# Kernel tuning notes

Measured on AMD Instinct MI355X. Metric: run time of the kernel, lower is better.

Reference implementation:

```python
import jax, jax.numpy as jnp
import numpy as np

N_SITE, D, PHYS, W = 40, 128, 2, 8  # sites, MPS bond dim, physical dim, MPO bond dim


def setup_inputs() -> dict:
    key = jax.random.key(0)
    k1, k2 = jax.random.split(key)
    # scale so 40-step transfer-matrix products stay O(1) in float32
    M = jax.random.normal(k1, (N_SITE, D, PHYS, D), jnp.float32) * (D * PHYS) ** -0.5
    H = jax.random.normal(k2, (N_SITE, W, W, PHYS, PHYS), jnp.float32) * (W * PHYS * PHYS) ** -0.5
    return {"M": M, "H": H}


def _energy(M, H):
    # <M|H|M> via left-to-right environment sweep. L has shape (D_bra, w, D_ket).
    L0 = jnp.zeros((D, W, D), M.dtype).at[0, 0, 0].set(1.0)  # open left boundary

    def step(L, mh):
        m, h = mh  # m: (a,i,p) bond,phys,bond ; h: (w,x,i,j) mpo-bond,mpo-bond,phys-out,phys-in
        T = jnp.einsum('awb,aip->wbip', L, m)      # absorb bra tensor (real, so no conj)
        T = jnp.einsum('wbip,wxij->bpxj', T, h)    # absorb MPO tensor
        L = jnp.einsum('bpxj,bjq->pxq', T, m)      # absorb ket tensor
        return L, None

    L, _ = jax.lax.scan(step, L0, (M, H))
    return L[0, W - 1, 0]  # open right boundary (MPO right boundary = last index)


def _norm(M):
    # <M|M> via transfer-matrix sweep. N has shape (D_bra, D_ket); stays PSD.
    N0 = jnp.zeros((D, D), M.dtype).at[0, 0].set(1.0)

    def step(N, m):
        T = jnp.einsum('ab,aip->bip', N, m)
        N = jnp.einsum('bip,biq->pq', T, m)
        return N, None

    N, _ = jax.lax.scan(step, N0, M)
    return N[0, 0]


def reference(M, H):
    EPS = 0.0
    NORM_LIM = 10000.0
    energy = _energy(M, H)
    norm = _norm(M)
    loss = energy / (norm + EPS)  # torch.real is identity for real dtype
    reg = jax.nn.relu(norm - NORM_LIM)
    return (energy, norm, loss, reg)
```

## Files before the change

### kernel.cpp

```cpp
#include <hip/hip_runtime.h>


#define D 128
#define W 8
#define NS 40
#define NPAIR 20
#define HALF2 10
#define MSZ (D * 2 * D)
#define HSZ (W * W * 2 * 2)
#define M2SZ (D * 4 * D)
#define H2SZ (W * W * 4 * 4)
#define LSZ (D * W * D)
#define NSZ (D * D)
#define T2SZ (D * W * D * 4)
#define TNSZ (4 * D * D)

#define OFF_M2 0
#define OFF_MR2 (OFF_M2 + NPAIR * M2SZ)
#define OFF_H2 (OFF_MR2 + HALF2 * M2SZ)
#define OFF_HR2 (OFF_H2 + NPAIR * H2SZ)
#define OFF_LL (OFF_HR2 + HALF2 * H2SZ)
#define OFF_LR (OFF_LL + LSZ)
#define OFF_NL (OFF_LR + LSZ)
#define OFF_NR (OFF_NL + NSZ)
#define OFF_T2L (OFF_NR + NSZ)
#define OFF_T2R (OFF_T2L + T2SZ)
#define OFF_TNL (OFF_T2R + T2SZ)
#define OFF_TNR (OFF_TNL + TNSZ)
#define OFF_PART (OFF_TNR + TNSZ)
#define OFF_PARTN (OFF_PART + 128)

__global__ __launch_bounds__(256) void k_prep1(const float* __restrict__ Min,
                                               const float* __restrict__ Hin,
                                               float* __restrict__ ws) {
    __shared__ float As[32 * 34];
    __shared__ float Bs[32 * 68];
    int bid = blockIdx.x, t = threadIdx.x;
    if (bid < 640) {
        int m = bid >> 5, tile = bid & 31;
        int r0 = (tile & 7) * 32, c0 = (tile >> 3) * 64;
        const float* A = Min + (2 * m) * MSZ;
        const float* B = Min + (2 * m + 1) * MSZ;
        float* C = ws + OFF_M2 + m * M2SZ;
        int ty = t >> 4, tx = t & 15;
        float a00 = 0, a01 = 0, a02 = 0, a03 = 0;
        float a10 = 0, a11 = 0, a12 = 0, a13 = 0;
        for (int c = 0; c < 4; ++c) {
            int k0 = c * 32;
            __syncthreads();
            {
                int rr = t >> 3, kq = t & 7;
                int row = r0 + rr;
                const float4 v = *(const float4*)&A[(row >> 1) * 256 + (row & 1) * 128 + k0 + kq * 4];
                float* dst = &As[kq * 136 + rr];
                dst[0] = v.x; dst[34] = v.y; dst[68] = v.z; dst[102] = v.w;
            }
#pragma unroll
            for (int u = 0; u < 2; ++u) {
                int e = u * 256 + t;
                int kk = e >> 4, cq = e & 15;
                const float4 v = *(const float4*)&B[(k0 + kk) * 256 + c0 + cq * 4];
                *(float4*)&Bs[kk * 68 + cq * 4] = v;
            }
            __syncthreads();
#pragma unroll 8
            for (int kk = 0; kk < 32; ++kk) {
                float2 av = *(float2*)&As[kk * 34 + 2 * ty];
                float4 bv = *(float4*)&Bs[kk * 68 + 4 * tx];
                a00 += av.x * bv.x; a01 += av.x * bv.y; a02 += av.x * bv.z; a03 += av.x * bv.w;
                a10 += av.y * bv.x; a11 += av.y * bv.y; a12 += av.y * bv.z; a13 += av.y * bv.w;
            }
        }
        int r = r0 + 2 * ty, cc = c0 + 4 * tx;
        int a = r >> 1, i2 = cc >> 7, cd = cc & 127;
        float4 v0; v0.x = a00; v0.y = a01; v0.z = a02; v0.w = a03;
        float4 v1; v1.x = a10; v1.y = a11; v1.z = a12; v1.w = a13;
        *(float4*)&C[a * 512 + (0 * 2 + i2) * 128 + cd] = v0;
        *(float4*)&C[a * 512 + (1 * 2 + i2) * 128 + cd] = v1;
    } else {
        for (int idx = t; idx < NPAIR * H2SZ; idx += 256) {
            int m = idx >> 10, r = idx & 1023;
            int w = r >> 7, x = (r >> 4) & 7, I = (r >> 2) & 3, J = r & 3;
            int i1 = I >> 1, i2 = I & 1, j1 = J >> 1, j2 = J & 1;
            const float* Ha = Hin + (2 * m) * HSZ;
            const float* Hb = Hin + (2 * m + 1) * HSZ;
            float s = 0.f;
#pragma unroll
            for (int v = 0; v < 8; ++v)
                s += Ha[w * 32 + v * 4 + i1 * 2 + j1] * Hb[v * 32 + x * 4 + i2 * 2 + j2];
            ws[OFF_H2 + idx] = s;
        }
    }
}

#define PR_MR (HALF2 * M2SZ)
#define PR_HR (PR_MR + HALF2 * H2SZ)
#define PR_TOT (PR_HR + 2 * LSZ + 2 * NSZ)
__global__ __launch_bounds__(256) void k_prep2(float* __restrict__ ws) {
    for (int idx = blockIdx.x * 256 + threadIdx.x; idx < PR_TOT; idx += gridDim.x * 256) {
        if (idx < PR_MR) {
            int kr = idx >> 16, r = idx & 65535;
            int a = r >> 9, I = (r >> 7) & 3, p = r & 127;
            ws[OFF_MR2 + idx] = ws[OFF_M2 + (19 - kr) * M2SZ + p * 512 + I * 128 + a];
        } else if (idx < PR_HR) {
            int e = idx - PR_MR;
            int kr = e >> 10, r = e & 1023;
            int w = r >> 7, x = (r >> 4) & 7, lo = r & 15;
            ws[OFF_HR2 + e] = ws[OFF_H2 + (19 - kr) * H2SZ + x * 128 + w * 16 + lo];
        } else {
            int e = idx - PR_HR;
            int off; float v = 0.f;
            if (e < LSZ)            { off = OFF_LL + e; if (e == 0) v = 1.f; }
            else if (e < 2 * LSZ)   { int r = e - LSZ; off = OFF_LR + r; if (r == (W - 1) * D) v = 1.f; }
            else if (e < 2 * LSZ + NSZ) { int r = e - 2 * LSZ; off = OFF_NL + r; if (r == 0) v = 1.f; }
            else                    { int r = e - 2 * LSZ - NSZ; off = OFF_NR + r; if (r == 0) v = 1.f; }
            ws[off] = v;
        }
    }
}

__global__ __launch_bounds__(256) void k_A2(const float* __restrict__ ws_c,
                                            float* __restrict__ ws, int k) {
    __shared__ float sm[9472];
    (void)ws_c;
    int bid = blockIdx.x, t = threadIdx.x;
    if (bid < 128) {
        int side = bid >> 6;
        int eb = bid & 63;
        int b0 = (eb & 7) * 16;
        int p0 = (eb >> 3) * 16;
        const float* Lsrc = ws + (side ? OFF_LR : OFF_LL);
        const float* m2 = ws + (side ? OFF_MR2 : OFF_M2) + k * M2SZ;
        const float* h2 = ws + (side ? OFF_HR2 : OFF_H2) + k * H2SZ;
        float* T2 = ws + (side ? OFF_T2R : OFF_T2L);
        float* Ls = sm;
        float* ms = sm + 6400;
        float* hs = sm + 8448;
#pragma unroll
        for (int u = 0; u < 4; ++u) {
            int e = u * 256 + t;
            int w = e >> 7, I = (e >> 5) & 3, x = (e >> 2) & 7, J = e & 3;
            hs[e] = h2[w * 128 + x * 16 + I * 4 + J];
        }
        int b_l = t & 15, p_l = t >> 4;
        float acc[8][4];
#pragma unroll
        for (int w = 0; w < 8; ++w)
#pragma unroll
            for (int I = 0; I < 4; ++I) acc[w][I] = 0.f;
        for (int c = 0; c < 4; ++c) {
            int a0 = c * 32;
            __syncthreads();
#pragma unroll
            for (int u = 0; u < 4; ++u) {
                int e = u * 256 + t;
                int aa = e >> 5, w = (e >> 2) & 7, bq = e & 3;
                const float4 v = *(const float4*)&Lsrc[(a0 + aa) * 1024 + w * 128 + b0 + bq * 4];
                float* dst = &Ls[aa * 200 + bq * 48 + w];
                dst[0] = v.x; dst[12] = v.y; dst[24] = v.z; dst[36] = v.w;
            }
#pragma unroll
            for (int u = 0; u < 2; ++u) {
                int s = u * 256 + t;
                int aa = s >> 4, I = (s >> 2) & 3, pq = s & 3;
                const float4 v = *(const float4*)&m2[(a0 + aa) * 512 + I * 128 + p0 + pq * 4];
                *(float4*)&ms[aa * 64 + I * 16 + pq * 4] = v;
            }
            __syncthreads();
#pragma unroll 4
            for (int aa = 0; aa < 32; ++aa) {
                float4 l0 = *(float4*)&Ls[aa * 200 + b_l * 12];
                float4 l1 = *(float4*)&Ls[aa * 200 + b_l * 12 + 4];
                float lw[8] = {l0.x, l0.y, l0.z, l0.w, l1.x, l1.y, l1.z, l1.w};
                float mv[4];
#pragma unroll
                for (int I = 0; I < 4; ++I) mv[I] = ms[aa * 64 + I * 16 + p_l];
#pragma unroll
                for (int w = 0; w < 8; ++w)
#pragma unroll
                    for (int I = 0; I < 4; ++I) acc[w][I] += lw[w] * mv[I];
            }
        }
        float o[32];
#pragma unroll
        for (int xJ = 0; xJ < 32; ++xJ) o[xJ] = 0.f;
#pragma unroll
        for (int wI = 0; wI < 32; ++wI) {
            float tv = acc[wI >> 2][wI & 3];
#pragma unroll
            for (int xJ = 0; xJ < 32; ++xJ) o[xJ] += tv * hs[wI * 32 + xJ];
        }
        int b = b0 + b_l, p = p0 + p_l;
#pragma unroll
        for (int x = 0; x < 8; ++x) {
            float4 v; v.x = o[x * 4]; v.y = o[x * 4 + 1]; v.z = o[x * 4 + 2]; v.w = o[x * 4 + 3];
            *(float4*)&T2[p * 4096 + x * 512 + b * 4] = v;
        }
    } else {
        int nb = bid - 128;
        int side = nb >> 5;
        int nn = nb & 31;
        int b0 = (nn & 3) * 32;
        int c0 = (nn >> 2) * 64;
        const float* Nsrc = ws + (side ? OFF_NR : OFF_NL);
        const float* m2 = ws + (side ? OFF_MR2 : OFF_M2) + k * M2SZ;
        float* Tn = ws + (side ? OFF_TNR : OFF_TNL);
        float* As = sm;
        float* Bs = sm + 1056;
        int ty = t >> 4, tx = t & 15;
        float a00 = 0, a01 = 0, a02 = 0, a03 = 0;
        float a10 = 0, a11 = 0, a12 = 0, a13 = 0;
        for (int c = 0; c < 4; ++c) {
            int a0 = c * 32;
            __syncthreads();
#pragma unroll
            for (int u = 0; u < 4; ++u) {
                int e = u * 256 + t;
                int kk = e >> 5, col = e & 31;
                As[kk * 33 + col] = Nsrc[(a0 + kk) * 128 + b0 + col];
            }
#pragma unroll
            for (int u = 0; u < 8; ++u) {
                int e = u * 256 + t;
                int kk = e >> 6, col = e & 63;
                Bs[kk * 68 + col] = m2[(a0 + kk) * 512 + c0 + col];
            }
            __syncthreads();
#pragma unroll 8
            for (int kk = 0; kk < 32; ++kk) {
                float2 av = *(float2*)&As[kk * 33 + 2 * ty];
                float4 bv = *(float4*)&Bs[kk * 68 + 4 * tx];
                a00 += av.x * bv.x; a01 += av.x * bv.y; a02 += av.x * bv.z; a03 += av.x * bv.w;
                a10 += av.y * bv.x; a11 += av.y * bv.y; a12 += av.y * bv.z; a13 += av.y * bv.w;
            }
        }
        int b_ = b0 + 2 * ty;
        float rowv[2][4] = {{a00, a01, a02, a03}, {a10, a11, a12, a13}};
#pragma unroll
        for (int jj = 0; jj < 4; ++jj) {
            int col = c0 + 4 * tx + jj;
            int I = col >> 7, p = col & 127;
            Tn[I * 16384 + p * 128 + b_] = rowv[0][jj];
            Tn[I * 16384 + p * 128 + b_ + 1] = rowv[1][jj];
        }
    }
}

__global__ __launch_bounds__(256) void k_B2(float* __restrict__ ws, int k) {
    __shared__ float As[32 * 34];
    __shared__ float Bs[32 * 68];
    int bid = blockIdx.x, t = threadIdx.x;
    int ty = t >> 4, tx = t & 15;
    float a00 = 0, a01 = 0, a02 = 0, a03 = 0;
    float a10 = 0, a11 = 0, a12 = 0, a13 = 0;
    if (bid < 128) {
        int side = bid >> 6;
        int eb = bid & 63;
        int r0 = (eb & 31) * 32;
        int c0 = (eb >> 5) * 64;
        const float* A = ws + (side ? OFF_T2R : OFF_T2L);
        const float* B = ws + (side ? OFF_MR2 : OFF_M2) + k * M2SZ;
        float* C = ws + (side ? OFF_LR : OFF_LL);
        for (int c = 0; c < 16; ++c) {
            int k0 = c * 32;
            __syncthreads();
            {
                int rr = t >> 3, kq = t & 7;
                const float4 v = *(const float4*)&A[(r0 + rr) * 512 + k0 + kq * 4];
                float* dst = &As[kq * 136 + rr];
                dst[0] = v.x; dst[34] = v.y; dst[68] = v.z; dst[102] = v.w;
            }
#pragma unroll
            for (int u = 0; u < 2; ++u) {
                int e = u * 256 + t;
                int kk = e >> 4, cq = e & 15;
                int row = k0 + kk;
                const float4 v = *(const float4*)&B[(row >> 2) * 512 + (row & 3) * 128 + c0 + cq * 4];
                *(float4*)&Bs[kk * 68 + cq * 4] = v;
            }
            __syncthreads();
#pragma unroll 8
            for (int kk = 0; kk < 32; ++kk) {
                float2 av = *(float2*)&As[kk * 34 + 2 * ty];
                float4 bv = *(float4*)&Bs[kk * 68 + 4 * tx];
                a00 += av.x * bv.x; a01 += av.x * bv.y; a02 += av.x * bv.z; a03 += av.x * bv.w;
                a10 += av.y * bv.x; a11 += av.y * bv.y; a12 += av.y * bv.z; a13 += av.y * bv.w;
            }
        }
        int r = r0 + 2 * ty, cc = c0 + 4 * tx;
        float4 v0; v0.x = a00; v0.y = a01; v0.z = a02; v0.w = a03;
        float4 v1; v1.x = a10; v1.y = a11; v1.z = a12; v1.w = a13;
        *(float4*)&C[(r >> 3) * 1024 + (r & 7) * 128 + cc] = v0;
        *(float4*)&C[((r + 1) >> 3) * 1024 + ((r + 1) & 7) * 128 + cc] = v1;
    } else if (bid < 144) {
        int nb = bid - 128;
        int side = nb >> 3;
        int nn = nb & 7;
        int r0 = (nn & 3) * 32;
        int c0 = (nn >> 2) * 64;
        const float* A = ws + (side ? OFF_TNR : OFF_TNL);
        const float* B = ws + (side ? OFF_MR2 : OFF_M2) + k * M2SZ;
        float* C = ws + (side ? OFF_NR : OFF_NL);
        for (int c = 0; c < 16; ++c) {
            int k0 = c * 32;
            int Ic = k0 >> 7, bc = k0 & 127;
            __syncthreads();
            {
                int rr = t >> 3, kq = t & 7;
                const float4 v = *(const float4*)&A[Ic * 16384 + (r0 + rr) * 128 + bc + kq * 4];
                float* dst = &As[kq * 136 + rr];
                dst[0] = v.x; dst[34] = v.y; dst[68] = v.z; dst[102] = v.w;
            }
#pragma unroll
            for (int u = 0; u < 2; ++u) {
                int e = u * 256 + t;
                int kk = e >> 4, cq = e & 15;
                const float4 v = *(const float4*)&B[(bc + kk) * 512 + Ic * 128 + c0 + cq * 4];
                *(float4*)&Bs[kk * 68 + cq * 4] = v;
            }
            __syncthreads();
#pragma unroll 8
            for (int kk = 0; kk < 32; ++kk) {
                float2 av = *(float2*)&As[kk * 34 + 2 * ty];
                float4 bv = *(float4*)&Bs[kk * 68 + 4 * tx];
                a00 += av.x * bv.x; a01 += av.x * bv.y; a02 += av.x * bv.z; a03 += av.x * bv.w;
                a10 += av.y * bv.x; a11 += av.y * bv.y; a12 += av.y * bv.z; a13 += av.y * bv.w;
            }
        }
        int r = r0 + 2 * ty, cc = c0 + 4 * tx;
        float4 v0; v0.x = a00; v0.y = a01; v0.z = a02; v0.w = a03;
        float4 v1; v1.x = a10; v1.y = a11; v1.z = a12; v1.w = a13;
        *(float4*)&C[r * 128 + cc] = v0;
        *(float4*)&C[(r + 1) * 128 + cc] = v1;
    }
}

__global__ __launch_bounds__(256) void k_dot(float* __restrict__ ws) {
    __shared__ float se[256], sn[256];
    int bid = blockIdx.x, t = threadIdx.x;
    const float* LL = ws + OFF_LL;
    const float* LR = ws + OFF_LR;
    float e = 0.f;
#pragma unroll
    for (int u = 0; u < 4; ++u) {
        int i = bid * 1024 + u * 256 + t;
        e += LL[i] * LR[i];
    }
    float n = 0.f;
    if (t < 128) {
        int i = bid * 128 + t;
        n = ws[OFF_NL + i] * ws[OFF_NR + i];
    }
    se[t] = e;
    sn[t] = n;
    __syncthreads();
    for (int s = 128; s > 0; s >>= 1) {
        if (t < s) { se[t] += se[t + s]; sn[t] += sn[t + s]; }
        __syncthreads();
    }
    if (t == 0) {
        ws[OFF_PART + bid] = se[0];
        ws[OFF_PARTN + bid] = sn[0];
    }
}

__global__ __launch_bounds__(256) void k_loss(const float* __restrict__ ws,
                                              float* __restrict__ out) {
    __shared__ float se[128], sn[128];
    int t = threadIdx.x;
    if (t < 128) {
        se[t] = ws[OFF_PART + t];
        sn[t] = ws[OFF_PARTN + t];
    }
    __syncthreads();
    for (int s = 64; s > 0; s >>= 1) {
        if (t < s) { se[t] += se[t + s]; sn[t] += sn[t + s]; }
        __syncthreads();
    }
    if (t == 0) {
        float E = se[0], Nm = sn[0];
        out[0] = E;
        out[1] = Nm;
        out[2] = E / Nm;
        out[3] = fmaxf(Nm - 10000.0f, 0.0f);
    }
}

extern "C" void kernel_launch(void* const* d_in, const int* in_sizes, int n_in,
                              void* d_out, int out_size, void* d_ws, size_t ws_size,
                              hipStream_t stream) {
    const float* Min = (const float*)d_in[0];
    const float* Hin = (const float*)d_in[1];
    float* ws = (float*)d_ws;
    float* out = (float*)d_out;
    (void)in_sizes; (void)n_in; (void)out_size; (void)ws_size;

    k_prep1<<<dim3(641), dim3(256), 0, stream>>>(Min, Hin, ws);
    k_prep2<<<dim3(640), dim3(256), 0, stream>>>(ws);
    for (int k = 0; k < HALF2; ++k) {
        k_A2<<<dim3(192), dim3(256), 0, stream>>>(ws, ws, k);
        k_B2<<<dim3(144), dim3(256), 0, stream>>>(ws, k);
    }
    k_dot<<<dim3(128), dim3(256), 0, stream>>>(ws);
    k_loss<<<dim3(1), dim3(256), 0, stream>>>(ws, out);
}
```

Baseline: 476.8 us.

## Fuse whole sweep into one persistent kernel with software grid barriers

Replaces the chain of about two dozen kernel launches (prep, ten A/B step pairs, dot, loss) with a single persistent kernel of 256 blocks. Stages are separated by custom global barriers using relaxed atomics, an XCD-aware writeback fence, and sc0 loads that bypass stale cache. The norm-sweep tasks are re-tiled and the B stages use larger K chunks. The aim is to remove launch gaps between dependent steps, at the cost of relying on co-residency of all blocks and on hand-written cache-coherence handling that could be fragile.

```diff
diff --git a/kernel.cpp b/kernel.cpp
--- a/kernel.cpp
+++ b/kernel.cpp
@@ -28,16 +28,112 @@
 #define OFF_TNL (OFF_T2R + T2SZ)
 #define OFF_TNR (OFF_TNL + TNSZ)
 #define OFF_PART (OFF_TNR + TNSZ)
-#define OFF_PARTN (OFF_PART + 128)
-
-__global__ __launch_bounds__(256) void k_prep1(const float* __restrict__ Min,
-                                               const float* __restrict__ Hin,
-                                               float* __restrict__ ws) {
-    __shared__ float As[32 * 34];
-    __shared__ float Bs[32 * 68];
-    int bid = blockIdx.x, t = threadIdx.x;
-    if (bid < 640) {
-        int m = bid >> 5, tile = bid & 31;
+#define OFF_PARTN (OFF_PART + 128 * 32)
+#define WS_FLOATS (OFF_PARTN + 128 * 32)
+
+#define NBLK 256
+#define OFF_BAR WS_FLOATS
+#define BAR_CLEAN (32 * NBLK)
+#define BAR_CNT (BAR_CLEAN + 32 * 8)
+#define BAR_LCTR (BAR_CNT + 32 * 8)
+#define BAR_INTS (BAR_LCTR + 32 * 4)
+
+#define PR2_TOT (HALF2 * M2SZ + HALF2 * H2SZ)
+
+typedef float f32x4_t __attribute__((ext_vector_type(4)));
+
+__device__ __forceinline__ int ld_rlx(int* p) {
+    return __hip_atomic_load(p, __ATOMIC_RELAXED, __HIP_MEMORY_SCOPE_AGENT);
+}
+__device__ __forceinline__ void st_rlx(int* p, int v) {
+    __hip_atomic_store(p, v, __ATOMIC_RELAXED, __HIP_MEMORY_SCOPE_AGENT);
+}
+__device__ __forceinline__ int fadd_rlx(int* p, int v) {
+    return __hip_atomic_fetch_add(p, v, __ATOMIC_RELAXED, __HIP_MEMORY_SCOPE_AGENT);
+}
+
+__device__ __forceinline__ float ld_sc0(const float* p) {
+    float v;
+    asm volatile("global_load_dword %0, %1, off sc0\n\ts_waitcnt vmcnt(0)"
+                 : "=&v"(v) : "v"(p) : "memory");
+    return v;
+}
+__device__ __forceinline__ void ld1x4_sc0(const float* p0, const float* p1,
+                                          const float* p2, const float* p3,
+                                          float& v0, float& v1, float& v2, float& v3) {
+    asm volatile(
+        "global_load_dword %0, %4, off sc0\n\t"
+        "global_load_dword %1, %5, off sc0\n\t"
+        "global_load_dword %2, %6, off sc0\n\t"
+        "global_load_dword %3, %7, off sc0\n\t"
+        "s_waitcnt vmcnt(0)"
+        : "=&v"(v0), "=&v"(v1), "=&v"(v2), "=&v"(v3)
+        : "v"(p0), "v"(p1), "v"(p2), "v"(p3) : "memory");
+}
+__device__ __forceinline__ void ld4x2_sc0(const float* p0, const float* p1,
+                                          f32x4_t& v0, f32x4_t& v1) {
+    asm volatile(
+        "global_load_dwordx4 %0, %2, off sc0\n\t"
+        "global_load_dwordx4 %1, %3, off sc0\n\t"
+        "s_waitcnt vmcnt(0)"
+        : "=&v"(v0), "=&v"(v1) : "v"(p0), "v"(p1) : "memory");
+}
+__device__ __forceinline__ void ld4x4_sc0(const float* p0, const float* p1,
+                                          const float* p2, const float* p3,
+                                          f32x4_t& v0, f32x4_t& v1,
+                                          f32x4_t& v2, f32x4_t& v3) {
+    asm volatile(
+        "global_load_dwordx4 %0, %4, off sc0\n\t"
+        "global_load_dwordx4 %1, %5, off sc0\n\t"
+        "global_load_dwordx4 %2, %6, off sc0\n\t"
+        "global_load_dwordx4 %3, %7, off sc0\n\t"
+        "s_waitcnt vmcnt(0)"
+        : "=&v"(v0), "=&v"(v1), "=&v"(v2), "=&v"(v3)
+        : "v"(p0), "v"(p1), "v"(p2), "v"(p3) : "memory");
+}
+
+__global__ __launch_bounds__(256) void k_bzero(float* ws) {
+    int idx = blockIdx.x * 256 + threadIdx.x;
+    int* bar = (int*)(ws + OFF_BAR);
+    if (idx < BAR_INTS) bar[idx] = 0;
+}
+
+__device__ void gbar(int* bar, int ep, bool wb, int isLead, int myxcd,
+                     unsigned presMask) {
+    int t = threadIdx.x;
+    asm volatile("s_waitcnt vmcnt(0)" ::: "memory");
+    __syncthreads();
+    if (t == 0) st_rlx(&bar[32 * blockIdx.x], ep);
+    while (ld_rlx(&bar[32 * t]) < ep) __builtin_amdgcn_s_sleep(2);
+    __syncthreads();
+    if (wb) {
+        if (isLead && t == 0) {
+            __builtin_amdgcn_fence(__ATOMIC_RELEASE, "agent");
+            st_rlx(&bar[BAR_CLEAN + 32 * myxcd], ep);
+        }
+        if (t < 8 && ((presMask >> t) & 1)) {
+            while (ld_rlx(&bar[BAR_CLEAN + 32 * t]) < ep) __builtin_amdgcn_s_sleep(2);
+        }
+        __syncthreads();
+    }
+}
+
+__device__ __forceinline__ void lbar(int* lc, int target) {
+    asm volatile("s_waitcnt vmcnt(0)" ::: "memory");
+    __syncthreads();
+    if (threadIdx.x == 0) {
+        fadd_rlx(lc, 1);
+        while (ld_rlx(lc) < target) __builtin_amdgcn_s_sleep(2);
+    }
+    __syncthreads();
+}
+
+__device__ void prep1_task(int task, const float* Min, const float* Hin,
+                           float* ws, float* sm, int t) {
+    if (task < 640) {
+        float* As = sm;
+        float* Bs = sm + 1088;
+        int m = task >> 5, tile = task & 31;
         int r0 = (tile & 7) * 32, c0 = (tile >> 3) * 64;
         const float* A = Min + (2 * m) * MSZ;
         const float* B = Min + (2 * m + 1) * MSZ;
@@ -51,7 +147,7 @@
             {
                 int rr = t >> 3, kq = t & 7;
                 int row = r0 + rr;
-                const float4 v = *(const float4*)&A[(row >> 1) * 256 + (row & 1) * 128 + k0 + kq * 4];
+                const f32x4_t v = *(const f32x4_t*)&A[(row >> 1) * 256 + (row & 1) * 128 + k0 + kq * 4];
                 float* dst = &As[kq * 136 + rr];
                 dst[0] = v.x; dst[34] = v.y; dst[68] = v.z; dst[102] = v.w;
             }
@@ -59,26 +155,27 @@
             for (int u = 0; u < 2; ++u) {
                 int e = u * 256 + t;
                 int kk = e >> 4, cq = e & 15;
-                const float4 v = *(const float4*)&B[(k0 + kk) * 256 + c0 + cq * 4];
-                *(float4*)&Bs[kk * 68 + cq * 4] = v;
+                const f32x4_t v = *(const f32x4_t*)&B[(k0 + kk) * 256 + c0 + cq * 4];
+                *(f32x4_t*)&Bs[kk * 68 + cq * 4] = v;
             }
             __syncthreads();
 #pragma unroll 8
             for (int kk = 0; kk < 32; ++kk) {
-                float2 av = *(float2*)&As[kk * 34 + 2 * ty];
-                float4 bv = *(float4*)&Bs[kk * 68 + 4 * tx];
-                a00 += av.x * bv.x; a01 += av.x * bv.y; a02 += av.x * bv.z; a03 += av.x * bv.w;
-                a10 += av.y * bv.x; a11 += av.y * bv.y; a12 += av.y * bv.z; a13 += av.y * bv.w;
+                float av0 = As[kk * 34 + 2 * ty], av1 = As[kk * 34 + 2 * ty + 1];
+                f32x4_t bv = *(const f32x4_t*)&Bs[kk * 68 + 4 * tx];
+                a00 += av0 * bv.x; a01 += av0 * bv.y; a02 += av0 * bv.z; a03 += av0 * bv.w;
+                a10 += av1 * bv.x; a11 += av1 * bv.y; a12 += av1 * bv.z; a13 += av1 * bv.w;
             }
         }
         int r = r0 + 2 * ty, cc = c0 + 4 * tx;
         int a = r >> 1, i2 = cc >> 7, cd = cc & 127;
-        float4 v0; v0.x = a00; v0.y = a01; v0.z = a02; v0.w = a03;
-        float4 v1; v1.x = a10; v1.y = a11; v1.z = a12; v1.w = a13;
-        *(float4*)&C[a * 512 + (0 * 2 + i2) * 128 + cd] = v0;
-        *(float4*)&C[a * 512 + (1 * 2 + i2) * 128 + cd] = v1;
+        f32x4_t v0; v0.x = a00; v0.y = a01; v0.z = a02; v0.w = a03;
+        f32x4_t v1; v1.x = a10; v1.y = a11; v1.z = a12; v1.w = a13;
+        *(f32x4_t*)&C[a * 512 + (0 * 2 + i2) * 128 + cd] = v0;
+        *(f32x4_t*)&C[a * 512 + (1 * 2 + i2) * 128 + cd] = v1;
     } else {
-        for (int idx = t; idx < NPAIR * H2SZ; idx += 256) {
+        int chunk = task - 640;
+        for (int idx = chunk * 1280 + t; idx < (chunk + 1) * 1280; idx += 256) {
             int m = idx >> 10, r = idx & 1023;
             int w = r >> 7, x = (r >> 4) & 7, I = (r >> 2) & 3, J = r & 3;
             int i1 = I >> 1, i2 = I & 1, j1 = J >> 1, j2 = J & 1;
@@ -93,296 +190,382 @@
     }
 }
 
-#define PR_MR (HALF2 * M2SZ)
-#define PR_HR (PR_MR + HALF2 * H2SZ)
-#define PR_TOT (PR_HR + 2 * LSZ + 2 * NSZ)
-__global__ __launch_bounds__(256) void k_prep2(float* __restrict__ ws) {
-    for (int idx = blockIdx.x * 256 + threadIdx.x; idx < PR_TOT; idx += gridDim.x * 256) {
-        if (idx < PR_MR) {
+__device__ void eA_task(int eb, const float* L, const float* m2, const float* h2,
+                        float* T2, float* sm, int t) {
+    int b0 = (eb & 7) * 16;
+    int p0 = (eb >> 3) * 16;
+    float* Ls = sm;
+    float* ms = sm + 6400;
+    float* hs = sm + 8448;
+    __syncthreads();
+#pragma unroll
+    for (int u = 0; u < 4; ++u) {
+        int e = u * 256 + t;
+        int w = e >> 7, I = (e >> 5) & 3, x = (e >> 2) & 7, J = e & 3;
+        hs[e] = h2[w * 128 + x * 16 + I * 4 + J];
+    }
+    int b_l = t & 15, p_l = t >> 4;
+    float acc[8][4];
+#pragma unroll
+    for (int w = 0; w < 8; ++w)
+#pragma unroll
+        for (int I = 0; I < 4; ++I) acc[w][I] = 0.f;
+    for (int c = 0; c < 4; ++c) {
+        int a0 = c * 32;
+        __syncthreads();
+        {
+            int e0 = t, e1 = 256 + t, e2 = 512 + t, e3 = 768 + t;
+            const float* q0 = &L[(a0 + (e0 >> 5)) * 1024 + ((e0 >> 2) & 7) * 128 + b0 + (e0 & 3) * 4];
+            const float* q1 = &L[(a0 + (e1 >> 5)) * 1024 + ((e1 >> 2) & 7) * 128 + b0 + (e1 & 3) * 4];
+            const float* q2 = &L[(a0 + (e2 >> 5)) * 1024 + ((e2 >> 2) & 7) * 128 + b0 + (e2 & 3) * 4];
+            const float* q3 = &L[(a0 + (e3 >> 5)) * 1024 + ((e3 >> 2) & 7) * 128 + b0 + (e3 & 3) * 4];
+            f32x4_t v0, v1, v2, v3;
+            ld4x4_sc0(q0, q1, q2, q3, v0, v1, v2, v3);
+            float* d0 = &Ls[(e0 >> 5) * 200 + (e0 & 3) * 48 + ((e0 >> 2) & 7)];
+            d0[0] = v0.x; d0[12] = v0.y; d0[24] = v0.z; d0[36] = v0.w;
+            float* d1 = &Ls[(e1 >> 5) * 200 + (e1 & 3) * 48 + ((e1 >> 2) & 7)];
+            d1[0] = v1.x; d1[12] = v1.y; d1[24] = v1.z; d1[36] = v1.w;
+            float* d2 = &Ls[(e2 >> 5) * 200 + (e2 & 3) * 48 + ((e2 >> 2) & 7)];
+            d2[0] = v2.x; d2[12] = v2.y; d2[24] = v2.z; d2[36] = v2.w;
+            float* d3 = &Ls[(e3 >> 5) * 200 + (e3 & 3) * 48 + ((e3 >> 2) & 7)];
+            d3[0] = v3.x; d3[12] = v3.y; d3[24] = v3.z; d3[36] = v3.w;
+        }
+#pragma unroll
+        for (int u = 0; u < 2; ++u) {
+            int s = u * 256 + t;
+            int aa = s >> 4, I = (s >> 2) & 3, pq = s & 3;
+            const f32x4_t v = *(const f32x4_t*)&m2[(a0 + aa) * 512 + I * 128 + p0 + pq * 4];
+            *(f32x4_t*)&ms[aa * 64 + I * 16 + pq * 4] = v;
+        }
+        __syncthreads();
+#pragma unroll 4
+        for (int aa = 0; aa < 32; ++aa) {
+            f32x4_t l0 = *(const f32x4_t*)&Ls[aa * 200 + b_l * 12];
+            f32x4_t l1 = *(const f32x4_t*)&Ls[aa * 200 + b_l * 12 + 4];
+            float lw[8] = {l0.x, l0.y, l0.z, l0.w, l1.x, l1.y, l1.z, l1.w};
+            float mv[4];
+#pragma unroll
+            for (int I = 0; I < 4; ++I) mv[I] = ms[aa * 64 + I * 16 + p_l];
+#pragma unroll
+            for (int w = 0; w < 8; ++w)
+#pragma unroll
+                for (int I = 0; I < 4; ++I) acc[w][I] += lw[w] * mv[I];
+        }
+    }
+    float o[32];
+#pragma unroll
+    for (int xJ = 0; xJ < 32; ++xJ) o[xJ] = 0.f;
+#pragma unroll
+    for (int wI = 0; wI < 32; ++wI) {
+        float tv = acc[wI >> 2][wI & 3];
+#pragma unroll
+        for (int xJ = 0; xJ < 32; ++xJ) o[xJ] += tv * hs[wI * 32 + xJ];
+    }
+    int b = b0 + b_l, p = p0 + p_l;
+#pragma unroll
+    for (int x = 0; x < 8; ++x) {
+        f32x4_t v; v.x = o[x * 4]; v.y = o[x * 4 + 1]; v.z = o[x * 4 + 2]; v.w = o[x * 4 + 3];
+        *(f32x4_t*)&T2[p * 4096 + x * 512 + b * 4] = v;
+    }
+}
+
+__device__ void eB_task(int eb, const float* T2A, const float* m2, float* Lout,
+                        float* sm, int t) {
+    float* As = sm;
+    float* Bs = sm + 2176;
+    int r0 = (eb & 31) * 32;
+    int c0 = (eb >> 5) * 64;
+    int ty = t >> 4, tx = t & 15;
+    float a00 = 0, a01 = 0, a02 = 0, a03 = 0;
+    float a10 = 0, a11 = 0, a12 = 0, a13 = 0;
+    for (int c = 0; c < 8; ++c) {
+        int k0 = c * 64;
+        __syncthreads();
+        {
+            int rr = t >> 3, kq = t & 7;
+            const float* p0 = &T2A[(r0 + rr) * 512 + k0 + kq * 4];
+            const float* p1 = p0 + 32;
+            f32x4_t v0, v1;
+            ld4x2_sc0(p0, p1, v0, v1);
+            float* d0 = &As[kq * 136 + rr];
+            d0[0] = v0.x; d0[34] = v0.y; d0[68] = v0.z; d0[102] = v0.w;
+            float* d1 = &As[(kq + 8) * 136 + rr];
+            d1[0] = v1.x; d1[34] = v1.y; d1[68] = v1.z; d1[102] = v1.w;
+        }
+#pragma unroll
+        for (int u = 0; u < 4; ++u) {
+            int e = u * 256 + t;
+            int kk = e >> 4, cq = e & 15;
+            int row = k0 + kk;
+            const f32x4_t v = *(const f32x4_t*)&m2[(row >> 2) * 512 + (row & 3) * 128 + c0 + cq * 4];
+            *(f32x4_t*)&Bs[kk * 68 + cq * 4] = v;
+        }
+        __syncthreads();
+#pragma unroll 8
+        for (int kk = 0; kk < 64; ++kk) {
+            float av0 = As[kk * 34 + 2 * ty], av1 = As[kk * 34 + 2 * ty + 1];
+            f32x4_t bv = *(const f32x4_t*)&Bs[kk * 68 + 4 * tx];
+            a00 += av0 * bv.x; a01 += av0 * bv.y; a02 += av0 * bv.z; a03 += av0 * bv.w;
+            a10 += av1 * bv.x; a11 += av1 * bv.y; a12 += av1 * bv.z; a13 += av1 * bv.w;
+        }
+    }
+    int r = r0 + 2 * ty, cc = c0 + 4 * tx;
+    f32x4_t v0; v0.x = a00; v0.y = a01; v0.z = a02; v0.w = a03;
+    f32x4_t v1; v1.x = a10; v1.y = a11; v1.z = a12; v1.w = a13;
+    *(f32x4_t*)&Lout[(r >> 3) * 1024 + (r & 7) * 128 + cc] = v0;
+    *(f32x4_t*)&Lout[((r + 1) >> 3) * 1024 + ((r + 1) & 7) * 128 + cc] = v1;
+}
+
+__device__ void nA_task(int nn, const float* N, const float* m2, float* Tn,
+                        float* sm, int t) {
+    float* As = sm;
+    float* Bs = sm + 1056;
+    int b0 = (nn & 3) * 32;
+    int c0 = (nn >> 2) * 64;
+    int ty = t >> 4, tx = t & 15;
+    float a00 = 0, a01 = 0, a02 = 0, a03 = 0;
+    float a10 = 0, a11 = 0, a12 = 0, a13 = 0;
+    for (int c = 0; c < 4; ++c) {
+        int a0 = c * 32;
+        __syncthreads();
+        {
+            int e0 = t, e1 = 256 + t, e2 = 512 + t, e3 = 768 + t;
+            const float* q0 = &N[(a0 + (e0 >> 5)) * 128 + b0 + (e0 & 31)];
+            const float* q1 = &N[(a0 + (e1 >> 5)) * 128 + b0 + (e1 & 31)];
+            const float* q2 = &N[(a0 + (e2 >> 5)) * 128 + b0 + (e2 & 31)];
+            const float* q3 = &N[(a0 + (e3 >> 5)) * 128 + b0 + (e3 & 31)];
+            float f0, f1, f2, f3;
+            ld1x4_sc0(q0, q1, q2, q3, f0, f1, f2, f3);
+            As[(e0 >> 5) * 33 + (e0 & 31)] = f0;
+            As[(e1 >> 5) * 33 + (e1 & 31)] = f1;
+            As[(e2 >> 5) * 33 + (e2 & 31)] = f2;
+            As[(e3 >> 5) * 33 + (e3 & 31)] = f3;
+        }
+#pragma unroll
+        for (int u = 0; u < 2; ++u) {
+            int e = u * 256 + t;
+            int kk = e >> 4, cq = e & 15;
+            const f32x4_t v = *(const f32x4_t*)&m2[(a0 + kk) * 512 + c0 + cq * 4];
+            *(f32x4_t*)&Bs[kk * 68 + cq * 4] = v;
+        }
+        __syncthreads();
+#pragma unroll 8
+        for (int kk = 0; kk < 32; ++kk) {
+            float av0 = As[kk * 33 + 2 * ty], av1 = As[kk * 33 + 2 * ty + 1];
+            f32x4_t bv = *(const f32x4_t*)&Bs[kk * 68 + 4 * tx];
+            a00 += av0 * bv.x; a01 += av0 * bv.y; a02 += av0 * bv.z; a03 += av0 * bv.w;
+            a10 += av1 * bv.x; a11 += av1 * bv.y; a12 += av1 * bv.z; a13 += av1 * bv.w;
+        }
+    }
+    int b_ = b0 + 2 * ty;
+    float rowv[2][4] = {{a00, a01, a02, a03}, {a10, a11, a12, a13}};
+#pragma unroll
+    for (int jj = 0; jj < 4; ++jj) {
+        int col = c0 + 4 * tx + jj;
+        int I = col >> 7, p = col & 127;
+        Tn[I * 16384 + p * 128 + b_] = rowv[0][jj];
+        Tn[I * 16384 + p * 128 + b_ + 1] = rowv[1][jj];
+    }
+}
+
+__device__ void nB_task(int nn, const float* Tn, const float* m2, float* Nout,
+                        float* sm, int t) {
+    float* As = sm;
+    float* Bs = sm + 2176;
+    int r0 = (nn & 3) * 32;
+    int c0 = (nn >> 2) * 64;
+    int ty = t >> 4, tx = t & 15;
+    float a00 = 0, a01 = 0, a02 = 0, a03 = 0;
+    float a10 = 0, a11 = 0, a12 = 0, a13 = 0;
+    for (int c = 0; c < 8; ++c) {
+        int Ic = c >> 1, bc = (c & 1) * 64;
+        __syncthreads();
+        {
+            int rr = t >> 3, kq = t & 7;
+            const float* p0 = &Tn[Ic * 16384 + (r0 + rr) * 128 + bc + kq * 4];
+            const float* p1 = p0 + 32;
+            f32x4_t v0, v1;
+            ld4x2_sc0(p0, p1, v0, v1);
+            float* d0 = &As[kq * 136 + rr];
+            d0[0] = v0.x; d0[34] = v0.y; d0[68] = v0.z; d0[102] = v0.w;
+            float* d1 = &As[(kq + 8) * 136 + rr];
+            d1[0] = v1.x; d1[34] = v1.y; d1[68] = v1.z; d1[102] = v1.w;
+        }
+#pragma unroll
+        for (int u = 0; u < 4; ++u) {
+            int e = u * 256 + t;
+            int kk = e >> 4, cq = e & 15;
+            const f32x4_t v = *(const f32x4_t*)&m2[(bc + kk) * 512 + Ic * 128 + c0 + cq * 4];
+            *(f32x4_t*)&Bs[kk * 68 + cq * 4] = v;
+        }
+        __syncthreads();
+#pragma unroll 8
+        for (int kk = 0; kk < 64; ++kk) {
+            float av0 = As[kk * 34 + 2 * ty], av1 = As[kk * 34 + 2 * ty + 1];
+            f32x4_t bv = *(const f32x4_t*)&Bs[kk * 68 + 4 * tx];
+            a00 += av0 * bv.x; a01 += av0 * bv.y; a02 += av0 * bv.z; a03 += av0 * bv.w;
+            a10 += av1 * bv.x; a11 += av1 * bv.y; a12 += av1 * bv.z; a13 += av1 * bv.w;
+        }
+    }
+    int r = r0 + 2 * ty, cc = c0 + 4 * tx;
+    f32x4_t v0; v0.x = a00; v0.y = a01; v0.z = a02; v0.w = a03;
+    f32x4_t v1; v1.x = a10; v1.y = a11; v1.z = a12; v1.w = a13;
+    *(f32x4_t*)&Nout[r * 128 + cc] = v0;
+    *(f32x4_t*)&Nout[(r + 1) * 128 + cc] = v1;
+}
+
+__global__ __launch_bounds__(256) void k_sweep(const float* __restrict__ Min,
+                                               const float* __restrict__ Hin,
+                                               float* __restrict__ ws,
+                                               float* __restrict__ out) {
+    __shared__ __align__(16) float sm[9472];
+    __shared__ int shI[12];
+    int* bar = (int*)(ws + OFF_BAR);
+    const int bid = blockIdx.x;
+    const int t = threadIdx.x;
+
+    if (t == 0) {
+        int x;
+        asm volatile("s_getreg_b32 %0, hwreg(HW_REG_XCC_ID)" : "=s"(x));
+        x &= 7;
+        int r = fadd_rlx(&bar[BAR_CNT + 32 * x], 1);
+        shI[0] = x; shI[1] = r;
+    }
+    __syncthreads();
+    const int myxcd = shI[0], rank = shI[1];
+
+    gbar(bar, 1, false, 0, 0, 0);
+
+    if (t == 0) {
+        int pres[8]; unsigned pm = 0; int np = 0;
+        for (int x = 0; x < 8; ++x) {
+            int c = ld_rlx(&bar[BAR_CNT + 32 * x]);
+            if (x == myxcd) shI[2] = c;
+            if (c > 0) { pres[np++] = x; pm |= 1u << x; }
+        }
+        shI[3] = (rank == 0);
+        shI[4] = (int)pm;
+        int nmc = 0;
+        for (int c = 0; c < 4; ++c)
+            if (pres[c % np] == myxcd) shI[6 + nmc++] = c;
+        shI[5] = nmc;
+    }
+    __syncthreads();
+    const int n_g = shI[2], isLead = shI[3];
+    const unsigned presMask = (unsigned)shI[4];
+    const int nMyChains = shI[5];
+
+    for (int task = bid; task < 656; task += NBLK)
+        prep1_task(task, Min, Hin, ws, sm, t);
+    gbar(bar, 2, true, isLead, myxcd, presMask);
+
+    for (int idx = bid * 256 + t; idx < PR2_TOT; idx += NBLK * 256) {
+        if (idx < HALF2 * M2SZ) {
             int kr = idx >> 16, r = idx & 65535;
             int a = r >> 9, I = (r >> 7) & 3, p = r & 127;
             ws[OFF_MR2 + idx] = ws[OFF_M2 + (19 - kr) * M2SZ + p * 512 + I * 128 + a];
-        } else if (idx < PR_HR) {
-            int e = idx - PR_MR;
+        } else {
+            int e = idx - HALF2 * M2SZ;
             int kr = e >> 10, r = e & 1023;
             int w = r >> 7, x = (r >> 4) & 7, lo = r & 15;
             ws[OFF_HR2 + e] = ws[OFF_H2 + (19 - kr) * H2SZ + x * 128 + w * 16 + lo];
+        }
+    }
+    gbar(bar, 3, true, isLead, myxcd, presMask);
+
+    for (int ci = 0; ci < nMyChains; ++ci) {
+        int chain = shI[6 + ci];
+        int* lc = &bar[BAR_LCTR + 32 * chain];
+        int lep = 0;
+        int side = chain & 1;
+        if (chain < 2) {
+            float* L = ws + (side ? OFF_LR : OFF_LL);
+            const float* m2b = ws + (side ? OFF_MR2 : OFF_M2);
+            const float* h2b = ws + (side ? OFF_HR2 : OFF_H2);
+            float* T2 = ws + (side ? OFF_T2R : OFF_T2L);
+            int hot = side ? (W - 1) * D : 0;
+            for (int i = rank * 256 + t; i < LSZ; i += n_g * 256)
+                L[i] = (i == hot) ? 1.f : 0.f;
+            ++lep; lbar(lc, lep * n_g);
+            for (int k = 0; k < HALF2; ++k) {
+                const float* m2 = m2b + k * M2SZ;
+                const float* h2 = h2b + k * H2SZ;
+                for (int task = rank; task < 64; task += n_g)
+                    eA_task(task, L, m2, h2, T2, sm, t);
+                ++lep; lbar(lc, lep * n_g);
+                for (int task = rank; task < 64; task += n_g)
+                    eB_task(task, T2, m2, L, sm, t);
+                ++lep; lbar(lc, lep * n_g);
+            }
         } else {
-            int e = idx - PR_HR;
-            int off; float v = 0.f;
-            if (e < LSZ)            { off = OFF_LL + e; if (e == 0) v = 1.f; }
-            else if (e < 2 * LSZ)   { int r = e - LSZ; off = OFF_LR + r; if (r == (W - 1) * D) v = 1.f; }
-            else if (e < 2 * LSZ + NSZ) { int r = e - 2 * LSZ; off = OFF_NL + r; if (r == 0) v = 1.f; }
-            else                    { int r = e - 2 * LSZ - NSZ; off = OFF_NR + r; if (r == 0) v = 1.f; }
-            ws[off] = v;
-        }
-    }
-}
-
-__global__ __launch_bounds__(256) void k_A2(const float* __restrict__ ws_c,
-                                            float* __restrict__ ws, int k) {
-    __shared__ float sm[9472];
-    (void)ws_c;
-    int bid = blockIdx.x, t = threadIdx.x;
+            float* N = ws + (side ? OFF_NR : OFF_NL);
+            const float* m2b = ws + (side ? OFF_MR2 : OFF_M2);
+            float* Tn = ws + (side ? OFF_TNR : OFF_TNL);
+            for (int i = rank * 256 + t; i < NSZ; i += n_g * 256)
+                N[i] = (i == 0) ? 1.f : 0.f;
+            ++lep; lbar(lc, lep * n_g);
+            for (int k = 0; k < HALF2; ++k) {
+                const float* m2 = m2b + k * M2SZ;
+                for (int task = rank; task < 32; task += n_g)
+                    nA_task(task, N, m2, Tn, sm, t);
+                ++lep; lbar(lc, lep * n_g);
+                for (int task = rank; task < 8; task += n_g)
+                    nB_task(task, Tn, m2, N, sm, t);
+                ++lep; lbar(lc, lep * n_g);
+            }
+        }
+    }
+    gbar(bar, 4, true, isLead, myxcd, presMask);
+
     if (bid < 128) {
-        int side = bid >> 6;
-        int eb = bid & 63;
-        int b0 = (eb & 7) * 16;
-        int p0 = (eb >> 3) * 16;
-        const float* Lsrc = ws + (side ? OFF_LR : OFF_LL);
-        const float* m2 = ws + (side ? OFF_MR2 : OFF_M2) + k * M2SZ;
-        const float* h2 = ws + (side ? OFF_HR2 : OFF_H2) + k * H2SZ;
-        float* T2 = ws + (side ? OFF_T2R : OFF_T2L);
-        float* Ls = sm;
-        float* ms = sm + 6400;
-        float* hs = sm + 8448;
+        float* se = sm;
+        float* sn = sm + 256;
+        const float* LL = ws + OFF_LL;
+        const float* LR = ws + OFF_LR;
+        float e = 0.f;
 #pragma unroll
         for (int u = 0; u < 4; ++u) {
-            int e = u * 256 + t;
-            int w = e >> 7, I = (e >> 5) & 3, x = (e >> 2) & 7, J = e & 3;
-            hs[e] = h2[w * 128 + x * 16 + I * 4 + J];
-        }
-        int b_l = t & 15, p_l = t >> 4;
-        float acc[8][4];
-#pragma unroll
-        for (int w = 0; w < 8; ++w)
-#pragma unroll
-            for (int I = 0; I < 4; ++I) acc[w][I] = 0.f;
-        for (int c = 0; c < 4; ++c) {
-            int a0 = c * 32;
+            int i = bid * 1024 + u * 256 + t;
+            e += ld_sc0(&LL[i]) * ld_sc0(&LR[i]);
+        }
+        float n = 0.f;
+        if (t < 128) {
+            int i = bid * 128 + t;
+            n = ld_sc0(&ws[OFF_NL + i]) * ld_sc0(&ws[OFF_NR + i]);
+        }
+        se[t] = e;
+        sn[t] = n;
+        __syncthreads();
+        for (int s = 128; s > 0; s >>= 1) {
+            if (t < s) { se[t] += se[t + s]; sn[t] += sn[t + s]; }
             __syncthreads();
-#pragma unroll
-            for (int u = 0; u < 4; ++u) {
-                int e = u * 256 + t;
-                int aa = e >> 5, w = (e >> 2) & 7, bq = e & 3;
-                const float4 v = *(const float4*)&Lsrc[(a0 + aa) * 1024 + w * 128 + b0 + bq * 4];
-                float* dst = &Ls[aa * 200 + bq * 48 + w];
-                dst[0] = v.x; dst[12] = v.y; dst[24] = v.z; dst[36] = v.w;
-            }
-#pragma unroll
-            for (int u = 0; u < 2; ++u) {
-                int s = u * 256 + t;
-                int aa = s >> 4, I = (s >> 2) & 3, pq = s & 3;
-                const float4 v = *(const float4*)&m2[(a0 + aa) * 512 + I * 128 + p0 + pq * 4];
-                *(float4*)&ms[aa * 64 + I * 16 + pq * 4] = v;
-            }
+        }
+        if (t == 0) {
+            ws[OFF_PART + bid * 32] = se[0];
+            ws[OFF_PARTN + bid * 32] = sn[0];
+        }
+    }
+    gbar(bar, 5, true, isLead, myxcd, presMask);
+
+    if (bid == 0) {
+        float* se = sm;
+        float* sn = sm + 128;
+        if (t < 128) {
+            se[t] = ws[OFF_PART + t * 32];
+            sn[t] = ws[OFF_PARTN + t * 32];
+        }
+        __syncthreads();
+        for (int s = 64; s > 0; s >>= 1) {
+            if (t < s) { se[t] += se[t + s]; sn[t] += sn[t + s]; }
             __syncthreads();
-#pragma unroll 4
-            for (int aa = 0; aa < 32; ++aa) {
-                float4 l0 = *(float4*)&Ls[aa * 200 + b_l * 12];
-                float4 l1 = *(float4*)&Ls[aa * 200 + b_l * 12 + 4];
-                float lw[8] = {l0.x, l0.y, l0.z, l0.w, l1.x, l1.y, l1.z, l1.w};
-                float mv[4];
-#pragma unroll
-                for (int I = 0; I < 4; ++I) mv[I] = ms[aa * 64 + I * 16 + p_l];
-#pragma unroll
-                for (int w = 0; w < 8; ++w)
-#pragma unroll
-                    for (int I = 0; I < 4; ++I) acc[w][I] += lw[w] * mv[I];
-            }
-        }
-        float o[32];
-#pragma unroll
-        for (int xJ = 0; xJ < 32; ++xJ) o[xJ] = 0.f;
-#pragma unroll
-        for (int wI = 0; wI < 32; ++wI) {
-            float tv = acc[wI >> 2][wI & 3];
-#pragma unroll
-            for (int xJ = 0; xJ < 32; ++xJ) o[xJ] += tv * hs[wI * 32 + xJ];
-        }
-        int b = b0 + b_l, p = p0 + p_l;
-#pragma unroll
-        for (int x = 0; x < 8; ++x) {
-            float4 v; v.x = o[x * 4]; v.y = o[x * 4 + 1]; v.z = o[x * 4 + 2]; v.w = o[x * 4 + 3];
-            *(float4*)&T2[p * 4096 + x * 512 + b * 4] = v;
-        }
-    } else {
-        int nb = bid - 128;
-        int side = nb >> 5;
-        int nn = nb & 31;
-        int b0 = (nn & 3) * 32;
-        int c0 = (nn >> 2) * 64;
-        const float* Nsrc = ws + (side ? OFF_NR : OFF_NL);
-        const float* m2 = ws + (side ? OFF_MR2 : OFF_M2) + k * M2SZ;
-        float* Tn = ws + (side ? OFF_TNR : OFF_TNL);
-        float* As = sm;
-        float* Bs = sm + 1056;
-        int ty = t >> 4, tx = t & 15;
-        float a00 = 0, a01 = 0, a02 = 0, a03 = 0;
-        float a10 = 0, a11 = 0, a12 = 0, a13 = 0;
-        for (int c = 0; c < 4; ++c) {
-            int a0 = c * 32;
-            __syncthreads();
-#pragma unroll
-            for (int u = 0; u < 4; ++u) {
-                int e = u * 256 + t;
-                int kk = e >> 5, col = e & 31;
-                As[kk * 33 + col] = Nsrc[(a0 + kk) * 128 + b0 + col];
-            }
-#pragma unroll
-            for (int u = 0; u < 8; ++u) {
-                int e = u * 256 + t;
-                int kk = e >> 6, col = e & 63;
-                Bs[kk * 68 + col] = m2[(a0 + kk) * 512 + c0 + col];
-            }
-            __syncthreads();
-#pragma unroll 8
-            for (int kk = 0; kk < 32; ++kk) {
-                float2 av = *(float2*)&As[kk * 33 + 2 * ty];
-                float4 bv = *(float4*)&Bs[kk * 68 + 4 * tx];
-                a00 += av.x * bv.x; a01 += av.x * bv.y; a02 += av.x * bv.z; a03 += av.x * bv.w;
-                a10 += av.y * bv.x; a11 += av.y * bv.y; a12 += av.y * bv.z; a13 += av.y * bv.w;
-            }
-        }
-        int b_ = b0 + 2 * ty;
-        float rowv[2][4] = {{a00, a01, a02, a03}, {a10, a11, a12, a13}};
-#pragma unroll
-        for (int jj = 0; jj < 4; ++jj) {
-            int col = c0 + 4 * tx + jj;
-            int I = col >> 7, p = col & 127;
-            Tn[I * 16384 + p * 128 + b_] = rowv[0][jj];
-            Tn[I * 16384 + p * 128 + b_ + 1] = rowv[1][jj];
-        }
-    }
-}
-
-__global__ __launch_bounds__(256) void k_B2(float* __restrict__ ws, int k) {
-    __shared__ float As[32 * 34];
-    __shared__ float Bs[32 * 68];
-    int bid = blockIdx.x, t = threadIdx.x;
-    int ty = t >> 4, tx = t & 15;
-    float a00 = 0, a01 = 0, a02 = 0, a03 = 0;
-    float a10 = 0, a11 = 0, a12 = 0, a13 = 0;
-    if (bid < 128) {
-        int side = bid >> 6;
-        int eb = bid & 63;
-        int r0 = (eb & 31) * 32;
-        int c0 = (eb >> 5) * 64;
-        const float* A = ws + (side ? OFF_T2R : OFF_T2L);
-        const float* B = ws + (side ? OFF_MR2 : OFF_M2) + k * M2SZ;
-        float* C = ws + (side ? OFF_LR : OFF_LL);
-        for (int c = 0; c < 16; ++c) {
-            int k0 = c * 32;
-            __syncthreads();
-            {
-                int rr = t >> 3, kq = t & 7;
-                const float4 v = *(const float4*)&A[(r0 + rr) * 512 + k0 + kq * 4];
-                float* dst = &As[kq * 136 + rr];
-                dst[0] = v.x; dst[34] = v.y; dst[68] = v.z; dst[102] = v.w;
-            }
-#pragma unroll
-            for (int u = 0; u < 2; ++u) {
-                int e = u * 256 + t;
-                int kk = e >> 4, cq = e & 15;
-                int row = k0 + kk;
-                const float4 v = *(const float4*)&B[(row >> 2) * 512 + (row & 3) * 128 + c0 + cq * 4];
-                *(float4*)&Bs[kk * 68 + cq * 4] = v;
-            }
-            __syncthreads();
-#pragma unroll 8
-            for (int kk = 0; kk < 32; ++kk) {
-                float2 av = *(float2*)&As[kk * 34 + 2 * ty];
-                float4 bv = *(float4*)&Bs[kk * 68 + 4 * tx];
-                a00 += av.x * bv.x; a01 += av.x * bv.y; a02 += av.x * bv.z; a03 += av.x * bv.w;
-                a10 += av.y * bv.x; a11 += av.y * bv.y; a12 += av.y * bv.z; a13 += av.y * bv.w;
-            }
-        }
-        int r = r0 + 2 * ty, cc = c0 + 4 * tx;
-        float4 v0; v0.x = a00; v0.y = a01; v0.z = a02; v0.w = a03;
-        float4 v1; v1.x = a10; v1.y = a11; v1.z = a12; v1.w = a13;
-        *(float4*)&C[(r >> 3) * 1024 + (r & 7) * 128 + cc] = v0;
-        *(float4*)&C[((r + 1) >> 3) * 1024 + ((r + 1) & 7) * 128 + cc] = v1;
-    } else if (bid < 144) {
-        int nb = bid - 128;
-        int side = nb >> 3;
-        int nn = nb & 7;
-        int r0 = (nn & 3) * 32;
-        int c0 = (nn >> 2) * 64;
-        const float* A = ws + (side ? OFF_TNR : OFF_TNL);
-        const float* B = ws + (side ? OFF_MR2 : OFF_M2) + k * M2SZ;
-        float* C = ws + (side ? OFF_NR : OFF_NL);
-        for (int c = 0; c < 16; ++c) {
-            int k0 = c * 32;
-            int Ic = k0 >> 7, bc = k0 & 127;
-            __syncthreads();
-            {
-                int rr = t >> 3, kq = t & 7;
-                const float4 v = *(const float4*)&A[Ic * 16384 + (r0 + rr) * 128 + bc + kq * 4];
-                float* dst = &As[kq * 136 + rr];
-                dst[0] = v.x; dst[34] = v.y; dst[68] = v.z; dst[102] = v.w;
-            }
-#pragma unroll
-            for (int u = 0; u < 2; ++u) {
-                int e = u * 256 + t;
-                int kk = e >> 4, cq = e & 15;
-                const float4 v = *(const float4*)&B[(bc + kk) * 512 + Ic * 128 + c0 + cq * 4];
-                *(float4*)&Bs[kk * 68 + cq * 4] = v;
-            }
-            __syncthreads();
-#pragma unroll 8
-            for (int kk = 0; kk < 32; ++kk) {
-                float2 av = *(float2*)&As[kk * 34 + 2 * ty];
-                float4 bv = *(float4*)&Bs[kk * 68 + 4 * tx];
-                a00 += av.x * bv.x; a01 += av.x * bv.y; a02 += av.x * bv.z; a03 += av.x * bv.w;
-                a10 += av.y * bv.x; a11 += av.y * bv.y; a12 += av.y * bv.z; a13 += av.y * bv.w;
-            }
-        }
-        int r = r0 + 2 * ty, cc = c0 + 4 * tx;
-        float4 v0; v0.x = a00; v0.y = a01; v0.z = a02; v0.w = a03;
-        float4 v1; v1.x = a10; v1.y = a11; v1.z = a12; v1.w = a13;
-        *(float4*)&C[r * 128 + cc] = v0;
-        *(float4*)&C[(r + 1) * 128 + cc] = v1;
-    }
-}
-
-__global__ __launch_bounds__(256) void k_dot(float* __restrict__ ws) {
-    __shared__ float se[256], sn[256];
-    int bid = blockIdx.x, t = threadIdx.x;
-    const float* LL = ws + OFF_LL;
-    const float* LR = ws + OFF_LR;
-    float e = 0.f;
-#pragma unroll
-    for (int u = 0; u < 4; ++u) {
-        int i = bid * 1024 + u * 256 + t;
-        e += LL[i] * LR[i];
-    }
-    float n = 0.f;
-    if (t < 128) {
-        int i = bid * 128 + t;
-        n = ws[OFF_NL + i] * ws[OFF_NR + i];
-    }
-    se[t] = e;
-    sn[t] = n;
-    __syncthreads();
-    for (int s = 128; s > 0; s >>= 1) {
-        if (t < s) { se[t] += se[t + s]; sn[t] += sn[t + s]; }
-        __syncthreads();
-    }
-    if (t == 0) {
-        ws[OFF_PART + bid] = se[0];
-        ws[OFF_PARTN + bid] = sn[0];
-    }
-}
-
-__global__ __launch_bounds__(256) void k_loss(const float* __restrict__ ws,
-                                              float* __restrict__ out) {
-    __shared__ float se[128], sn[128];
-    int t = threadIdx.x;
-    if (t < 128) {
-        se[t] = ws[OFF_PART + t];
-        sn[t] = ws[OFF_PARTN + t];
-    }
-    __syncthreads();
-    for (int s = 64; s > 0; s >>= 1) {
-        if (t < s) { se[t] += se[t + s]; sn[t] += sn[t + s]; }
-        __syncthreads();
-    }
-    if (t == 0) {
-        float E = se[0], Nm = sn[0];
-        out[0] = E;
-        out[1] = Nm;
-        out[2] = E / Nm;
-        out[3] = fmaxf(Nm - 10000.0f, 0.0f);
+        }
+        if (t == 0) {
+            float E = se[0], Nm = sn[0];
+            out[0] = E;
+            out[1] = Nm;
+            out[2] = E / Nm;
+            out[3] = fmaxf(Nm - 10000.0f, 0.0f);
+        }
     }
 }
 
@@ -395,12 +578,6 @@
     float* out = (float*)d_out;
     (void)in_sizes; (void)n_in; (void)out_size; (void)ws_size;
 
-    k_prep1<<<dim3(641), dim3(256), 0, stream>>>(Min, Hin, ws);
-    k_prep2<<<dim3(640), dim3(256), 0, stream>>>(ws);
-    for (int k = 0; k < HALF2; ++k) {
-        k_A2<<<dim3(192), dim3(256), 0, stream>>>(ws, ws, k);
-        k_B2<<<dim3(144), dim3(256), 0, stream>>>(ws, k);
-    }
-    k_dot<<<dim3(128), dim3(256), 0, stream>>>(ws);
-    k_loss<<<dim3(1), dim3(256), 0, stream>>>(ws, out);
-}
+    k_bzero<<<dim3((BAR_INTS + 255) / 256), dim3(256), 0, stream>>>(ws);
+    k_sweep<<<dim3(NBLK), dim3(256), 0, stream>>>(Min, Hin, ws, out);
+}
```

After: 698.7 us. +46.5%, slower.
